# Optimization experiments

Hardware: AMD Instinct MI355X
Metric: run time of the kernel (lower is better)

## Reference

```python
import jax, jax.numpy as jnp
import numpy as np

NUM_TILES = 512
N_POINTS = 512
D_IN = 256
D_OUT = 256
CHANNELS = 1024


def setup_inputs() -> dict:
    key = jax.random.key(0)
    k1, k2, k3 = jax.random.split(key, 3)
    x = jax.random.normal(k1, (NUM_TILES, N_POINTS, D_IN), dtype=jnp.float32)
    indices = jax.random.randint(k2, (NUM_TILES,), 0, CHANNELS, dtype=jnp.int64)
    # kaiming-uniform-like init for the per-channel weight tiles
    bound = float(np.sqrt(6.0 / D_IN))
    weight = jax.random.uniform(k3, (CHANNELS, D_IN, D_OUT), dtype=jnp.float32,
                                minval=-bound, maxval=bound)
    bias = jnp.zeros((1, 1, D_OUT), dtype=jnp.float32)
    return {"x": x, "indices": indices, "weight": weight, "bias": bias}


def reference(x, indices, weight, bias):
    # gather per-tile weights [T, D_in, D_out], then batched matmul
    w = weight[indices]  # [T, D_in, D_out]
    # [T, P, D_in] @ [T, D_in, D_out] -> [T, P, D_out]
    out = jnp.einsum('tpi,tio->tpo', x, w) + bias[0]
    return out
```

## Files before the change

kernel.cpp:

```cpp
#include <hip/hip_runtime.h>
#include <hip/hip_bf16.h>

typedef __attribute__((ext_vector_type(8))) short bf16x8;
typedef __attribute__((ext_vector_type(4))) short bf16x4;
typedef __attribute__((ext_vector_type(4))) float f32x4;

constexpr int NT   = 512;
constexpr int NP   = 512;
constexpr int DIN  = 256;
constexpr int DOUT = 256;
constexpr int CHM  = 64;

__device__ __forceinline__ short f2bf(float f) {
  __hip_bfloat16 h = __float2bfloat16(f);
  return __builtin_bit_cast(short, h);
}

__device__ __forceinline__ void wg_barrier() {
  asm volatile("s_waitcnt lgkmcnt(0)" ::: "memory");
  __builtin_amdgcn_s_barrier();
  __builtin_amdgcn_sched_barrier(0);
}

__device__ __forceinline__ int wsw(int n, int k) {
  return n * DIN + (k ^ (((n ^ (n >> 2)) & 7) << 3));
}

__device__ __forceinline__ int xsw(int m, int k) {
  return m * DIN + (k ^ ((m & 7) << 3));
}

__global__ __launch_bounds__(512, 2) void adaptive_linear_v7(
    const float* __restrict__ x,
    const int*   __restrict__ idx,
    const float* __restrict__ w,
    const float* __restrict__ bias,
    float*       __restrict__ out)
{
  __shared__ short Ws[DOUT * DIN];
  __shared__ short Xs[CHM * DIN];

  const int tid = threadIdx.x;
  const int t   = blockIdx.x;

  const int c = idx[t];
  const float* xb = x   + (size_t)t * NP * DIN;
  const float* wb = w   + (size_t)c * DIN * DOUT;
  float*       ob = out + (size_t)t * NP * DOUT;

  const int wl = tid & 63;
  const int wv = tid >> 6;
  f32x4 wr[8];

  auto load_w = [&](int ss) {
    const float* ws = wb + (size_t)(ss * 64 + wv * 8) * DOUT + wl * 4;
    #pragma unroll
    for (int q = 0; q < 8; ++q)
      wr[q] = *reinterpret_cast<const f32x4*>(ws + (size_t)q * DOUT);
  };
  auto write_w = [&](int ss) {
    #pragma unroll
    for (int h = 0; h < 2; ++h) {
      const int k0 = ss * 64 + wv * 8 + h * 4;
      #pragma unroll
      for (int j = 0; j < 4; ++j) {
        bf16x4 v = { f2bf(wr[h*4+0][j]), f2bf(wr[h*4+1][j]),
                     f2bf(wr[h*4+2][j]), f2bf(wr[h*4+3][j]) };
        *reinterpret_cast<bf16x4*>(&Ws[wsw(wl * 4 + j, k0)]) = v;
      }
    }
  };

  f32x4 xr[8];
  auto load_x = [&](int ch) {
    const float* base = xb + (size_t)ch * CHM * DIN;
    #pragma unroll
    for (int i = 0; i < 8; ++i)
      xr[i] = *reinterpret_cast<const f32x4*>(base + i * 2048 + tid * 4);
  };
  auto write_x = [&]() {
    const int m0 = tid >> 6;
    const int k  = (tid & 63) * 4;
    #pragma unroll
    for (int i = 0; i < 8; ++i) {
      bf16x4 v = { f2bf(xr[i][0]), f2bf(xr[i][1]),
                   f2bf(xr[i][2]), f2bf(xr[i][3]) };
      *reinterpret_cast<bf16x4*>(&Xs[xsw(m0 + i * 8, k)]) = v;
    }
  };

  const int l    = tid & 63;
  const int wid  = tid >> 6;
  const int wm   = wid >> 2;
  const int wn   = wid & 3;
  const int lrow = l & 15;
  const int lk   = l >> 4;

  float bv[4];
  #pragma unroll
  for (int fn = 0; fn < 4; ++fn)
    bv[fn] = bias[wn * 64 + fn * 16 + lrow];

  load_x(0);
  load_w(0);
  write_w(0);
  load_w(1); write_w(1);
  load_w(2); write_w(2);
  load_w(3); write_w(3);
  write_x();
  wg_barrier();

  for (int ch = 0; ch < 8; ++ch) {
    if (ch < 7) load_x(ch + 1);

    f32x4 acc[2][4] = {};
    #pragma unroll
    for (int ks = 0; ks < 8; ++ks) {
      const int kb = ks * 32 + lk * 8;
      bf16x8 a[2], b[4];
      #pragma unroll
      for (int fm = 0; fm < 2; ++fm)
        a[fm] = *reinterpret_cast<const bf16x8*>(
            &Xs[xsw(wm * 32 + fm * 16 + lrow, kb)]);
      #pragma unroll
      for (int fn = 0; fn < 4; ++fn)
        b[fn] = *reinterpret_cast<const bf16x8*>(
            &Ws[wsw(wn * 64 + fn * 16 + lrow, kb)]);
      #pragma unroll
      for (int fm = 0; fm < 2; ++fm)
        #pragma unroll
        for (int fn = 0; fn < 4; ++fn)
          acc[fm][fn] = __builtin_amdgcn_mfma_f32_16x16x32_bf16(
              a[fm], b[fn], acc[fm][fn], 0, 0, 0);
    }

    #pragma unroll
    for (int fm = 0; fm < 2; ++fm) {
      const int r0w = ch * CHM + wm * 32 + fm * 16 + lk * 4;
      #pragma unroll
      for (int fn = 0; fn < 4; ++fn) {
        const int col = wn * 64 + fn * 16 + lrow;
        float* op = ob + (size_t)r0w * DOUT + col;
        #pragma unroll
        for (int rr = 0; rr < 4; ++rr)
          op[(size_t)rr * DOUT] = acc[fm][fn][rr] + bv[fn];
      }
    }

    if (ch < 7) {
      wg_barrier();
      write_x();
      wg_barrier();
    }
  }
}

extern "C" void kernel_launch(void* const* d_in, const int* in_sizes, int n_in,
                              void* d_out, int out_size, void* d_ws, size_t ws_size,
                              hipStream_t stream) {
  const float* x    = (const float*)d_in[0];
  const int*   idx  = (const int*)d_in[1];
  const float* w    = (const float*)d_in[2];
  const float* bias = (const float*)d_in[3];
  float* out = (float*)d_out;

  adaptive_linear_v7<<<NT, 512, 0, stream>>>(x, idx, w, bias, out);
}
```

Measured before the change: 135.0 us.

## Split waves into producer and consumer roles with double-buffered X tiles

Each workgroup's eight waves are split in two. Four producer waves load and convert the next 32-row X chunk into one of two LDS buffers, and four consumer waves run the MFMA work on the current buffer and store the output. This replaces the load/barrier/write/barrier sequence with one barrier per chunk, so the global X load can overlap compute. In exchange only half the waves issue MFMAs, the chunks are smaller (more iterations), and the extra LDS buffer could limit occupancy.

```diff
diff --git a/kernel.cpp b/kernel.cpp
--- a/kernel.cpp
+++ b/kernel.cpp
@@ -9,7 +9,8 @@
 constexpr int NP   = 512;
 constexpr int DIN  = 256;
 constexpr int DOUT = 256;
-constexpr int CHM  = 64;
+constexpr int CHM  = 32;
+constexpr int NEP  = NP / CHM;
 
 __device__ __forceinline__ short f2bf(float f) {
   __hip_bfloat16 h = __float2bfloat16(f);
@@ -30,7 +31,7 @@
   return m * DIN + (k ^ ((m & 7) << 3));
 }
 
-__global__ __launch_bounds__(512, 2) void adaptive_linear_v7(
+__global__ __launch_bounds__(512, 2) void adaptive_linear_v8(
     const float* __restrict__ x,
     const int*   __restrict__ idx,
     const float* __restrict__ w,
@@ -38,7 +39,7 @@
     float*       __restrict__ out)
 {
   __shared__ short Ws[DOUT * DIN];
-  __shared__ short Xs[CHM * DIN];
+  __shared__ short Xs[2][CHM * DIN];
 
   const int tid = threadIdx.x;
   const int t   = blockIdx.x;
@@ -48,10 +49,12 @@
   const float* wb = w   + (size_t)c * DIN * DOUT;
   float*       ob = out + (size_t)t * NP * DOUT;
 
+  const int l   = tid & 63;
+  const int wid = tid >> 6;
+
   const int wl = tid & 63;
   const int wv = tid >> 6;
   f32x4 wr[8];
-
   auto load_w = [&](int ss) {
     const float* ws = wb + (size_t)(ss * 64 + wv * 8) * DOUT + wl * 4;
     #pragma unroll
@@ -71,87 +74,85 @@
     }
   };
 
+  const bool producer = (wid < 4);
+  const int  p = wid;
+  const int  q = wid - 4;
+
   f32x4 xr[8];
   auto load_x = [&](int ch) {
-    const float* base = xb + (size_t)ch * CHM * DIN;
+    const float* base = xb + (size_t)ch * CHM * DIN + (size_t)(p * 8) * DIN + l * 4;
     #pragma unroll
     for (int i = 0; i < 8; ++i)
-      xr[i] = *reinterpret_cast<const f32x4*>(base + i * 2048 + tid * 4);
+      xr[i] = *reinterpret_cast<const f32x4*>(base + (size_t)i * DIN);
   };
-  auto write_x = [&]() {
-    const int m0 = tid >> 6;
-    const int k  = (tid & 63) * 4;
+  auto write_x = [&](int b) {
     #pragma unroll
     for (int i = 0; i < 8; ++i) {
       bf16x4 v = { f2bf(xr[i][0]), f2bf(xr[i][1]),
                    f2bf(xr[i][2]), f2bf(xr[i][3]) };
-      *reinterpret_cast<bf16x4*>(&Xs[xsw(m0 + i * 8, k)]) = v;
+      *reinterpret_cast<bf16x4*>(&Xs[b][xsw(p * 8 + i, l * 4)]) = v;
     }
   };
 
-  const int l    = tid & 63;
-  const int wid  = tid >> 6;
-  const int wm   = wid >> 2;
-  const int wn   = wid & 3;
   const int lrow = l & 15;
   const int lk   = l >> 4;
+  float bv[4];
+  if (!producer) {
+    #pragma unroll
+    for (int fn = 0; fn < 4; ++fn)
+      bv[fn] = bias[q * 64 + fn * 16 + lrow];
+  }
 
-  float bv[4];
-  #pragma unroll
-  for (int fn = 0; fn < 4; ++fn)
-    bv[fn] = bias[wn * 64 + fn * 16 + lrow];
-
-  load_x(0);
-  load_w(0);
-  write_w(0);
+  if (producer) load_x(0);
+  load_w(0); write_w(0);
   load_w(1); write_w(1);
   load_w(2); write_w(2);
   load_w(3); write_w(3);
-  write_x();
+  if (producer) write_x(0);
   wg_barrier();
 
-  for (int ch = 0; ch < 8; ++ch) {
-    if (ch < 7) load_x(ch + 1);
-
-    f32x4 acc[2][4] = {};
-    #pragma unroll
-    for (int ks = 0; ks < 8; ++ks) {
-      const int kb = ks * 32 + lk * 8;
-      bf16x8 a[2], b[4];
+  for (int ch = 0; ch < NEP; ++ch) {
+    if (producer) {
+      if (ch < NEP - 1) {
+        load_x(ch + 1);
+        write_x((ch + 1) & 1);
+      }
+    } else {
+      f32x4 acc[2][4] = {};
+      const short* xbuf = Xs[ch & 1];
       #pragma unroll
-      for (int fm = 0; fm < 2; ++fm)
-        a[fm] = *reinterpret_cast<const bf16x8*>(
-            &Xs[xsw(wm * 32 + fm * 16 + lrow, kb)]);
-      #pragma unroll
-      for (int fn = 0; fn < 4; ++fn)
-        b[fn] = *reinterpret_cast<const bf16x8*>(
-            &Ws[wsw(wn * 64 + fn * 16 + lrow, kb)]);
-      #pragma unroll
-      for (int fm = 0; fm < 2; ++fm)
+      for (int ks = 0; ks < 8; ++ks) {
+        const int kb = ks * 32 + lk * 8;
+        bf16x8 a[2], b[4];
+        #pragma unroll
+        for (int fm = 0; fm < 2; ++fm)
+          a[fm] = *reinterpret_cast<const bf16x8*>(
+              &xbuf[xsw(fm * 16 + lrow, kb)]);
         #pragma unroll
         for (int fn = 0; fn < 4; ++fn)
-          acc[fm][fn] = __builtin_amdgcn_mfma_f32_16x16x32_bf16(
-              a[fm], b[fn], acc[fm][fn], 0, 0, 0);
-    }
-
-    #pragma unroll
-    for (int fm = 0; fm < 2; ++fm) {
-      const int r0w = ch * CHM + wm * 32 + fm * 16 + lk * 4;
+          b[fn] = *reinterpret_cast<const bf16x8*>(
+              &Ws[wsw(q * 64 + fn * 16 + lrow, kb)]);
+        #pragma unroll
+        for (int fm = 0; fm < 2; ++fm)
+          #pragma unroll
+          for (int fn = 0; fn < 4; ++fn)
+            acc[fm][fn] = __builtin_amdgcn_mfma_f32_16x16x32_bf16(
+                a[fm], b[fn], acc[fm][fn], 0, 0, 0);
+      }
       #pragma unroll
-      for (int fn = 0; fn < 4; ++fn) {
-        const int col = wn * 64 + fn * 16 + lrow;
-        float* op = ob + (size_t)r0w * DOUT + col;
+      for (int fm = 0; fm < 2; ++fm) {
+        const int r0w = ch * CHM + fm * 16 + lk * 4;
         #pragma unroll
-        for (int rr = 0; rr < 4; ++rr)
-          op[(size_t)rr * DOUT] = acc[fm][fn][rr] + bv[fn];
+        for (int fn = 0; fn < 4; ++fn) {
+          const int col = q * 64 + fn * 16 + lrow;
+          float* op = ob + (size_t)r0w * DOUT + col;
+          #pragma unroll
+          for (int rr = 0; rr < 4; ++rr)
+            op[(size_t)rr * DOUT] = acc[fm][fn][rr] + bv[fn];
+        }
       }
     }
-
-    if (ch < 7) {
-      wg_barrier();
-      write_x();
-      wg_barrier();
-    }
+    if (ch < NEP - 1) wg_barrier();
   }
 }
 
@@ -164,5 +165,5 @@
   const float* bias = (const float*)d_in[3];
   float* out = (float*)d_out;
 
-  adaptive_linear_v7<<<NT, 512, 0, stream>>>(x, idx, w, bias, out);
+  adaptive_linear_v8<<<NT, 512, 0, stream>>>(x, idx, w, bias, out);
 }
```

Result: faster. 131.9 us (-2.3%).

## Load x operands directly from global into registers, drop LDS staging of x

Applied to the files above, without the earlier changes.

Removes the shared-memory staging buffer for x and its per-chunk barriers. Each wave now loads its own 32 rows of x straight from global memory into registers, triple-buffered across k-steps, and converts them to bf16 in-register. Each wave covers all 256 output columns with 32 accumulators, and the kernel runs over two 256-row halves. MFMA sections get raised wave priority. This saves LDS traffic and synchronisation, at the cost of higher register pressure and less coalesced global loads of x.

```diff
diff --git a/kernel.cpp b/kernel.cpp
--- a/kernel.cpp
+++ b/kernel.cpp
@@ -9,28 +9,24 @@
 constexpr int NP   = 512;
 constexpr int DIN  = 256;
 constexpr int DOUT = 256;
-constexpr int CHM  = 64;
 
 __device__ __forceinline__ short f2bf(float f) {
   __hip_bfloat16 h = __float2bfloat16(f);
   return __builtin_bit_cast(short, h);
 }
 
-__device__ __forceinline__ void wg_barrier() {
-  asm volatile("s_waitcnt lgkmcnt(0)" ::: "memory");
-  __builtin_amdgcn_s_barrier();
-  __builtin_amdgcn_sched_barrier(0);
+__device__ __forceinline__ bf16x8 cvt8(f32x4 a, f32x4 b) {
+  bf16x8 r;
+  r[0] = f2bf(a[0]); r[1] = f2bf(a[1]); r[2] = f2bf(a[2]); r[3] = f2bf(a[3]);
+  r[4] = f2bf(b[0]); r[5] = f2bf(b[1]); r[6] = f2bf(b[2]); r[7] = f2bf(b[3]);
+  return r;
 }
 
 __device__ __forceinline__ int wsw(int n, int k) {
   return n * DIN + (k ^ (((n ^ (n >> 2)) & 7) << 3));
 }
 
-__device__ __forceinline__ int xsw(int m, int k) {
-  return m * DIN + (k ^ ((m & 7) << 3));
-}
-
-__global__ __launch_bounds__(512, 2) void adaptive_linear_v7(
+__global__ __launch_bounds__(512, 2) void adaptive_linear_v9(
     const float* __restrict__ x,
     const int*   __restrict__ idx,
     const float* __restrict__ w,
@@ -38,7 +34,6 @@
     float*       __restrict__ out)
 {
   __shared__ short Ws[DOUT * DIN];
-  __shared__ short Xs[CHM * DIN];
 
   const int tid = threadIdx.x;
   const int t   = blockIdx.x;
@@ -48,109 +43,103 @@
   const float* wb = w   + (size_t)c * DIN * DOUT;
   float*       ob = out + (size_t)t * NP * DOUT;
 
-  const int wl = tid & 63;
-  const int wv = tid >> 6;
-  f32x4 wr[8];
-
-  auto load_w = [&](int ss) {
-    const float* ws = wb + (size_t)(ss * 64 + wv * 8) * DOUT + wl * 4;
-    #pragma unroll
-    for (int q = 0; q < 8; ++q)
-      wr[q] = *reinterpret_cast<const f32x4*>(ws + (size_t)q * DOUT);
-  };
-  auto write_w = [&](int ss) {
-    #pragma unroll
-    for (int h = 0; h < 2; ++h) {
-      const int k0 = ss * 64 + wv * 8 + h * 4;
+  {
+    const int wl = tid & 63;
+    const int wv = tid >> 6;
+    f32x4 wr[8];
+    #pragma unroll 1
+    for (int ss = 0; ss < 4; ++ss) {
+      const float* ws = wb + (size_t)(ss * 64 + wv * 8) * DOUT + wl * 4;
       #pragma unroll
-      for (int j = 0; j < 4; ++j) {
-        bf16x4 v = { f2bf(wr[h*4+0][j]), f2bf(wr[h*4+1][j]),
-                     f2bf(wr[h*4+2][j]), f2bf(wr[h*4+3][j]) };
-        *reinterpret_cast<bf16x4*>(&Ws[wsw(wl * 4 + j, k0)]) = v;
+      for (int q = 0; q < 8; ++q)
+        wr[q] = *reinterpret_cast<const f32x4*>(ws + (size_t)q * DOUT);
+      #pragma unroll
+      for (int h = 0; h < 2; ++h) {
+        const int k0 = ss * 64 + wv * 8 + h * 4;
+        #pragma unroll
+        for (int j = 0; j < 4; ++j) {
+          bf16x4 v = { f2bf(wr[h*4+0][j]), f2bf(wr[h*4+1][j]),
+                       f2bf(wr[h*4+2][j]), f2bf(wr[h*4+3][j]) };
+          *reinterpret_cast<bf16x4*>(&Ws[wsw(wl * 4 + j, k0)]) = v;
+        }
       }
     }
-  };
-
-  f32x4 xr[8];
-  auto load_x = [&](int ch) {
-    const float* base = xb + (size_t)ch * CHM * DIN;
-    #pragma unroll
-    for (int i = 0; i < 8; ++i)
-      xr[i] = *reinterpret_cast<const f32x4*>(base + i * 2048 + tid * 4);
-  };
-  auto write_x = [&]() {
-    const int m0 = tid >> 6;
-    const int k  = (tid & 63) * 4;
-    #pragma unroll
-    for (int i = 0; i < 8; ++i) {
-      bf16x4 v = { f2bf(xr[i][0]), f2bf(xr[i][1]),
-                   f2bf(xr[i][2]), f2bf(xr[i][3]) };
-      *reinterpret_cast<bf16x4*>(&Xs[xsw(m0 + i * 8, k)]) = v;
-    }
-  };
+  }
+  __syncthreads();
 
   const int l    = tid & 63;
   const int wid  = tid >> 6;
-  const int wm   = wid >> 2;
-  const int wn   = wid & 3;
   const int lrow = l & 15;
   const int lk   = l >> 4;
 
-  float bv[4];
-  #pragma unroll
-  for (int fn = 0; fn < 4; ++fn)
-    bv[fn] = bias[wn * 64 + fn * 16 + lrow];
+  #pragma unroll 1
+  for (int half = 0; half < 2; ++half) {
+    const int rows = half * 256 + wid * 32;
+    const float* xs0 = xb + (size_t)rows * DIN;
 
-  load_x(0);
-  load_w(0);
-  write_w(0);
-  load_w(1); write_w(1);
-  load_w(2); write_w(2);
-  load_w(3); write_w(3);
-  write_x();
-  wg_barrier();
+    f32x4 acc[2][16];
+    #pragma unroll
+    for (int fm = 0; fm < 2; ++fm)
+      #pragma unroll
+      for (int fn = 0; fn < 16; ++fn)
+        acc[fm][fn] = f32x4{0.f, 0.f, 0.f, 0.f};
 
-  for (int ch = 0; ch < 8; ++ch) {
-    if (ch < 7) load_x(ch + 1);
+    f32x4 ar[3][2][2];
+    #define LOADA(KS, BUF)                                                   \
+      {                                                                      \
+        const float* p0 = xs0 + (size_t)lrow * DIN + (KS) * 32 + lk * 8;     \
+        _Pragma("unroll")                                                    \
+        for (int fm = 0; fm < 2; ++fm) {                                     \
+          const float* p = p0 + (size_t)fm * 16 * DIN;                       \
+          ar[BUF][fm][0] = *reinterpret_cast<const f32x4*>(p);               \
+          ar[BUF][fm][1] = *reinterpret_cast<const f32x4*>(p + 4);           \
+        }                                                                    \
+      }
 
-    f32x4 acc[2][4] = {};
+    LOADA(0, 0)
+    LOADA(1, 1)
+
     #pragma unroll
     for (int ks = 0; ks < 8; ++ks) {
-      const int kb = ks * 32 + lk * 8;
-      bf16x8 a[2], b[4];
+      if (ks < 6) LOADA(ks + 2, (ks + 2) % 3)
+
+      bf16x8 a[2];
       #pragma unroll
       for (int fm = 0; fm < 2; ++fm)
-        a[fm] = *reinterpret_cast<const bf16x8*>(
-            &Xs[xsw(wm * 32 + fm * 16 + lrow, kb)]);
+        a[fm] = cvt8(ar[ks % 3][fm][0], ar[ks % 3][fm][1]);
+
+      const int kb = ks * 32 + lk * 8;
+      __builtin_amdgcn_s_setprio(1);
       #pragma unroll
-      for (int fn = 0; fn < 4; ++fn)
-        b[fn] = *reinterpret_cast<const bf16x8*>(
-            &Ws[wsw(wn * 64 + fn * 16 + lrow, kb)]);
-      #pragma unroll
-      for (int fm = 0; fm < 2; ++fm)
+      for (int g = 0; g < 4; ++g) {
+        bf16x8 b[4];
         #pragma unroll
-        for (int fn = 0; fn < 4; ++fn)
-          acc[fm][fn] = __builtin_amdgcn_mfma_f32_16x16x32_bf16(
-              a[fm], b[fn], acc[fm][fn], 0, 0, 0);
+        for (int j = 0; j < 4; ++j)
+          b[j] = *reinterpret_cast<const bf16x8*>(
+              &Ws[wsw((g * 4 + j) * 16 + lrow, kb)]);
+        #pragma unroll
+        for (int fm = 0; fm < 2; ++fm)
+          #pragma unroll
+          for (int j = 0; j < 4; ++j)
+            acc[fm][g * 4 + j] = __builtin_amdgcn_mfma_f32_16x16x32_bf16(
+                a[fm], b[j], acc[fm][g * 4 + j], 0, 0, 0);
+      }
+      __builtin_amdgcn_s_setprio(0);
     }
+    #undef LOADA
 
     #pragma unroll
     for (int fm = 0; fm < 2; ++fm) {
-      const int r0w = ch * CHM + wm * 32 + fm * 16 + lk * 4;
+      const int r0w = rows + fm * 16 + lk * 4;
       #pragma unroll
-      for (int fn = 0; fn < 4; ++fn) {
-        const int col = wn * 64 + fn * 16 + lrow;
+      for (int fn = 0; fn < 16; ++fn) {
+        const int col = fn * 16 + lrow;
+        const float bv = bias[col];
         float* op = ob + (size_t)r0w * DOUT + col;
         #pragma unroll
         for (int rr = 0; rr < 4; ++rr)
-          op[(size_t)rr * DOUT] = acc[fm][fn][rr] + bv[fn];
+          op[(size_t)rr * DOUT] = acc[fm][fn][rr] + bv;
       }
-    }
-
-    if (ch < 7) {
-      wg_barrier();
-      write_x();
-      wg_barrier();
     }
   }
 }
@@ -164,5 +153,5 @@
   const float* bias = (const float*)d_in[3];
   float* out = (float*)d_out;
 
-  adaptive_linear_v7<<<NT, 512, 0, stream>>>(x, idx, w, bias, out);
+  adaptive_linear_v9<<<NT, 512, 0, stream>>>(x, idx, w, bias, out);
 }
```

Measured after the change: 205.5 us. 52.2% more time.

## Split each tile's output columns across two blocks with smaller row chunks

Applied to the files above, without the earlier changes.

Launches two blocks per tile, each owning 128 output columns. Each block stages only its half of the weight tile in LDS and processes rows in 32-row chunks. This cuts LDS per block and doubles the grid, aiming for more resident blocks and better latency hiding. The cost is that both halves read the full fp32 x slab, roughly doubling x traffic unless the paired blocks hit in cache. Each wave now issues fewer MFMAs per staged chunk.

```diff
diff --git a/kernel.cpp b/kernel.cpp
--- a/kernel.cpp
+++ b/kernel.cpp
@@ -9,7 +9,9 @@
 constexpr int NP   = 512;
 constexpr int DIN  = 256;
 constexpr int DOUT = 256;
-constexpr int CHM  = 64;
+constexpr int BN   = 128;
+constexpr int CHM  = 32;
+constexpr int NEP  = NP / CHM;
 
 __device__ __forceinline__ short f2bf(float f) {
   __hip_bfloat16 h = __float2bfloat16(f);
@@ -30,59 +32,58 @@
   return m * DIN + (k ^ ((m & 7) << 3));
 }
 
-__global__ __launch_bounds__(512, 2) void adaptive_linear_v7(
+__global__ __launch_bounds__(512, 4) void adaptive_linear_v12(
     const float* __restrict__ x,
     const int*   __restrict__ idx,
     const float* __restrict__ w,
     const float* __restrict__ bias,
     float*       __restrict__ out)
 {
-  __shared__ short Ws[DOUT * DIN];
+  __shared__ short Ws[BN * DIN];
   __shared__ short Xs[CHM * DIN];
 
   const int tid = threadIdx.x;
-  const int t   = blockIdx.x;
+  const int b   = blockIdx.x;
+  const int t   = (b >> 4) * 8 + (b & 7);
+  const int nh  = (b >> 3) & 1;
 
   const int c = idx[t];
   const float* xb = x   + (size_t)t * NP * DIN;
-  const float* wb = w   + (size_t)c * DIN * DOUT;
-  float*       ob = out + (size_t)t * NP * DOUT;
+  const float* wb = w   + (size_t)c * DIN * DOUT + nh * BN;
+  float*       ob = out + (size_t)t * NP * DOUT + nh * BN;
 
-  const int wl = tid & 63;
-  const int wv = tid >> 6;
-  f32x4 wr[8];
-
-  auto load_w = [&](int ss) {
-    const float* ws = wb + (size_t)(ss * 64 + wv * 8) * DOUT + wl * 4;
-    #pragma unroll
-    for (int q = 0; q < 8; ++q)
-      wr[q] = *reinterpret_cast<const f32x4*>(ws + (size_t)q * DOUT);
-  };
-  auto write_w = [&](int ss) {
-    #pragma unroll
-    for (int h = 0; h < 2; ++h) {
-      const int k0 = ss * 64 + wv * 8 + h * 4;
+  {
+    const int n4 = (tid & 31) * 4;
+    const int kg = tid >> 5;
+    f32x4 wr[4];
+    #pragma unroll 1
+    for (int ss = 0; ss < 4; ++ss) {
+      const int k0 = ss * 64 + kg * 4;
+      const float* src = wb + (size_t)k0 * DOUT + n4;
+      #pragma unroll
+      for (int r = 0; r < 4; ++r)
+        wr[r] = *reinterpret_cast<const f32x4*>(src + (size_t)r * DOUT);
       #pragma unroll
       for (int j = 0; j < 4; ++j) {
-        bf16x4 v = { f2bf(wr[h*4+0][j]), f2bf(wr[h*4+1][j]),
-                     f2bf(wr[h*4+2][j]), f2bf(wr[h*4+3][j]) };
-        *reinterpret_cast<bf16x4*>(&Ws[wsw(wl * 4 + j, k0)]) = v;
+        bf16x4 v = { f2bf(wr[0][j]), f2bf(wr[1][j]),
+                     f2bf(wr[2][j]), f2bf(wr[3][j]) };
+        *reinterpret_cast<bf16x4*>(&Ws[wsw(n4 + j, k0)]) = v;
       }
     }
-  };
+  }
 
-  f32x4 xr[8];
-  auto load_x = [&](int ch) {
-    const float* base = xb + (size_t)ch * CHM * DIN;
+  f32x4 xr[4];
+  auto load_x = [&](int e) {
+    const float* base = xb + (size_t)e * CHM * DIN;
     #pragma unroll
-    for (int i = 0; i < 8; ++i)
+    for (int i = 0; i < 4; ++i)
       xr[i] = *reinterpret_cast<const f32x4*>(base + i * 2048 + tid * 4);
   };
   auto write_x = [&]() {
     const int m0 = tid >> 6;
     const int k  = (tid & 63) * 4;
     #pragma unroll
-    for (int i = 0; i < 8; ++i) {
+    for (int i = 0; i < 4; ++i) {
       bf16x4 v = { f2bf(xr[i][0]), f2bf(xr[i][1]),
                    f2bf(xr[i][2]), f2bf(xr[i][3]) };
       *reinterpret_cast<bf16x4*>(&Xs[xsw(m0 + i * 8, k)]) = v;
@@ -96,58 +97,51 @@
   const int lrow = l & 15;
   const int lk   = l >> 4;
 
-  float bv[4];
+  float bv[2];
   #pragma unroll
-  for (int fn = 0; fn < 4; ++fn)
-    bv[fn] = bias[wn * 64 + fn * 16 + lrow];
+  for (int fn = 0; fn < 2; ++fn)
+    bv[fn] = bias[nh * BN + wn * 32 + fn * 16 + lrow];
 
   load_x(0);
-  load_w(0);
-  write_w(0);
-  load_w(1); write_w(1);
-  load_w(2); write_w(2);
-  load_w(3); write_w(3);
   write_x();
   wg_barrier();
 
-  for (int ch = 0; ch < 8; ++ch) {
-    if (ch < 7) load_x(ch + 1);
+  for (int e = 0; e < NEP; ++e) {
+    if (e < NEP - 1) load_x(e + 1);
 
-    f32x4 acc[2][4] = {};
+    f32x4 acc[2][2] = {};
     #pragma unroll
     for (int ks = 0; ks < 8; ++ks) {
       const int kb = ks * 32 + lk * 8;
-      bf16x8 a[2], b[4];
+      bf16x8 a[2], bb[2];
       #pragma unroll
       for (int fm = 0; fm < 2; ++fm)
         a[fm] = *reinterpret_cast<const bf16x8*>(
-            &Xs[xsw(wm * 32 + fm * 16 + lrow, kb)]);
+            &Xs[xsw(wm * 16 + fm * 8, kb)]);
+      a[0] = *reinterpret_cast<const bf16x8*>(&Xs[xsw(wm * 16 + lrow, kb)]);
       #pragma unroll
-      for (int fn = 0; fn < 4; ++fn)
-        b[fn] = *reinterpret_cast<const bf16x8*>(
-            &Ws[wsw(wn * 64 + fn * 16 + lrow, kb)]);
+      for (int fn = 0; fn < 2; ++fn)
+        bb[fn] = *reinterpret_cast<const bf16x8*>(
+            &Ws[wsw(wn * 32 + fn * 16 + lrow, kb)]);
       #pragma unroll
-      for (int fm = 0; fm < 2; ++fm)
-        #pragma unroll
-        for (int fn = 0; fn < 4; ++fn)
-          acc[fm][fn] = __builtin_amdgcn_mfma_f32_16x16x32_bf16(
-              a[fm], b[fn], acc[fm][fn], 0, 0, 0);
+      for (int fn = 0; fn < 2; ++fn)
+        acc[0][fn] = __builtin_amdgcn_mfma_f32_16x16x32_bf16(
+            a[0], bb[fn], acc[0][fn], 0, 0, 0);
     }
 
-    #pragma unroll
-    for (int fm = 0; fm < 2; ++fm) {
-      const int r0w = ch * CHM + wm * 32 + fm * 16 + lk * 4;
+    {
+      const int r0w = e * CHM + wm * 16 + lk * 4;
       #pragma unroll
-      for (int fn = 0; fn < 4; ++fn) {
-        const int col = wn * 64 + fn * 16 + lrow;
+      for (int fn = 0; fn < 2; ++fn) {
+        const int col = wn * 32 + fn * 16 + lrow;
         float* op = ob + (size_t)r0w * DOUT + col;
         #pragma unroll
         for (int rr = 0; rr < 4; ++rr)
-          op[(size_t)rr * DOUT] = acc[fm][fn][rr] + bv[fn];
+          op[(size_t)rr * DOUT] = acc[0][fn][rr] + bv[fn];
       }
     }
 
-    if (ch < 7) {
+    if (e < NEP - 1) {
       wg_barrier();
       write_x();
       wg_barrier();
@@ -164,5 +158,5 @@
   const float* bias = (const float*)d_in[3];
   float* out = (float*)d_out;
 
-  adaptive_linear_v7<<<NT, 512, 0, stream>>>(x, idx, w, bias, out);
+  adaptive_linear_v12<<<NT * 2, 512, 0, stream>>>(x, idx, w, bias, out);
 }
```

New measurement: 145.6 us. 7.8% more time.
